# Performance work log

Hardware: AMD Instinct MI355X
Metric: run time of the kernel (lower is better)

## Reference

```python
import jax, jax.numpy as jnp
import numpy as np

N = 100000      # num nodes
E = 1600000     # num edges
DIN, DH, DOUT = 128, 64, 32
BN_EPS = 1e-5


def setup_inputs() -> dict:
    key = jax.random.key(0)
    ks = jax.random.split(key, 6)

    def xavier(k, fi, fo):
        lim = np.sqrt(6.0 / (fi + fo)).astype(np.float32)
        return jax.random.uniform(k, (fi, fo), jnp.float32, -lim, lim)

    return {
        "x": jax.random.normal(ks[0], (N, DIN), jnp.float32),
        "edge_index": jax.random.randint(ks[1], (2, E), 0, N, dtype=jnp.int32),
        "W1": xavier(ks[2], DIN, DH),
        "b1": jnp.zeros((DH,), jnp.float32),
        "gamma1": jnp.ones((DH,), jnp.float32),
        "beta1": jnp.zeros((DH,), jnp.float32),
        "W2": xavier(ks[3], DH, DOUT),
        "b2": jnp.zeros((DOUT,), jnp.float32),
    }


def _gcn_norm(edge_index, n, dtype):
    # add self-loops, then symmetric normalization deg^-1/2[src] * deg^-1/2[dst]
    loop = jnp.arange(n, dtype=edge_index.dtype)
    src = jnp.concatenate([edge_index[0], loop])
    dst = jnp.concatenate([edge_index[1], loop])
    deg = jax.ops.segment_sum(jnp.ones_like(dst, dtype=dtype), dst, num_segments=n)
    dis = 1.0 / jnp.sqrt(deg)  # deg >= 1 due to self-loops
    norm = dis[src] * dis[dst]
    return src, dst, norm


def _gcn_layer(h, W, b, src, dst, norm, n):
    h = h @ W
    msg = h[src] * norm[:, None]                       # [E+N, d] gather
    out = jax.ops.segment_sum(msg, dst, num_segments=n)  # scatter-add
    return out + b


def reference(x, edge_index, W1, b1, gamma1, beta1, W2, b2):
    src, dst, norm = _gcn_norm(edge_index, N, x.dtype)
    # layer 1: GCNConv -> BatchNorm (batch stats) -> ReLU (dropout = eval/identity)
    h = _gcn_layer(x, W1, b1, src, dst, norm, N)
    mean = h.mean(axis=0)
    var = h.var(axis=0)
    h = (h - mean) / jnp.sqrt(var + BN_EPS) * gamma1 + beta1
    h = jax.nn.relu(h)
    # layer 2: GCNConv -> node embeddings [N, DOUT]
    out = _gcn_layer(h, W2, b2, src, dst, norm, N)
    return out
```

## Files before the change

kernel.cpp:

```cpp
#include <hip/hip_runtime.h>

#define DIN 128
#define DH 64
#define DOUT 32
#define BN_EPS 1e-5f

#define BK 128
#define BKSH 7
#define NBK_MAX 784
#define G 256
#define CAP 2560
#define CCAP 3584

typedef __attribute__((ext_vector_type(8))) short short8;
typedef __attribute__((ext_vector_type(4))) float floatx4;

__device__ __forceinline__ unsigned short f2bf(float f) {
    union { float f; unsigned u; } v; v.f = f;
    unsigned r = (v.u + 0x7FFFu + ((v.u >> 16) & 1u)) >> 16;
    return (unsigned short)r;
}
__device__ __forceinline__ float bf2f(unsigned short h) {
    union { unsigned u; float f; } v; v.u = ((unsigned)h) << 16;
    return v.f;
}
__device__ __forceinline__ float lo_f(unsigned u) {
    union { unsigned u; float f; } v; v.u = u << 16;
    return v.f;
}
__device__ __forceinline__ float hi_f(unsigned u) {
    union { unsigned u; float f; } v; v.u = u & 0xFFFF0000u;
    return v.f;
}
__device__ __forceinline__ unsigned pack2bf(float lo, float hi) {
    return (unsigned)f2bf(lo) | ((unsigned)f2bf(hi) << 16);
}


__global__ __launch_bounds__(512) void hist_k(const int* __restrict__ dst, int* __restrict__ hist_g,
                                              int E, int nbk, int chunk) {
    __shared__ int hist[NBK_MAX];
    int g = blockIdx.x, tid = threadIdx.x;
    for (int b = tid; b < nbk; b += 512) hist[b] = 0;
    __syncthreads();
    int i0 = g * chunk, iend = min(i0 + chunk, E);
    for (int i = i0 + tid; i < iend; i += 512)
        atomicAdd(&hist[dst[i] >> BKSH], 1);
    __syncthreads();
    for (int b = tid; b < nbk; b += 512)
        hist_g[(size_t)g * nbk + b] = hist[b];
}


__global__ __launch_bounds__(256) void scan_k(const int* __restrict__ hist_g, int* __restrict__ rowoff,
                                              int* __restrict__ tot, int nbk) {
    __shared__ int seg[16][17];
    int tid = threadIdx.x;
    int gl = tid >> 4, bl = tid & 15;
    int b = blockIdx.x * 16 + bl;
    bool bok = b < nbk;
    int vals[16];
    int psum = 0;
    #pragma unroll
    for (int j = 0; j < 16; j++) {
        int g = gl * 16 + j;
        int v = bok ? hist_g[(size_t)g * nbk + b] : 0;
        vals[j] = v; psum += v;
    }
    seg[gl][bl] = psum;
    __syncthreads();
    #pragma unroll
    for (int off = 1; off < 16; off <<= 1) {
        int t = (gl >= off) ? seg[gl - off][bl] : 0;
        __syncthreads();
        seg[gl][bl] += t;
        __syncthreads();
    }
    int run = seg[gl][bl] - psum;
    if (gl == 15 && bok) tot[b] = seg[15][bl];
    #pragma unroll
    for (int j = 0; j < 16; j++) {
        int g = gl * 16 + j;
        if (bok) rowoff[(size_t)g * nbk + b] = run;
        run += vals[j];
    }
}


__global__ __launch_bounds__(512) void scatter_k(const int* __restrict__ src, const int* __restrict__ dst,
                                                 const int* __restrict__ rowoff,
                                                 unsigned* __restrict__ recs, int E, int nbk, int chunk) {
    __shared__ int cur[NBK_MAX];
    int g = blockIdx.x, tid = threadIdx.x;
    for (int b = tid; b < nbk; b += 512)
        cur[b] = b * CAP + rowoff[(size_t)g * nbk + b];
    __syncthreads();
    int i0 = g * chunk, iend = min(i0 + chunk, E);
    for (int i = i0 + tid; i < iend; i += 512) {
        int s = src[i], d = dst[i];
        int b = d >> BKSH;
        int slot = atomicAdd(&cur[b], 1);
        if (slot < (b + 1) * CAP)
            recs[slot] = ((unsigned)s << BKSH) | (unsigned)(d & (BK - 1));
    }
}


__global__ __launch_bounds__(512) void csr_k(const unsigned* __restrict__ recs, const int* __restrict__ tot,
                                             float* __restrict__ dis, int2* __restrict__ rpde,
                                             int* __restrict__ col, int n) {
    __shared__ int deg8[8][BK];
    __shared__ int wb[8][BK];
    __shared__ int deg[BK], sc[BK], bas[BK];
    int b = blockIdx.x, tid = threadIdx.x;
    int w = tid >> 6, lane = tid & 63;
    for (int i = tid; i < 8 * BK; i += 512) ((int*)deg8)[i] = 0;
    __syncthreads();
    int lo = b * CAP;
    int clo = b * CCAP;
    int ne = min(tot[b], CAP);
    int hi = lo + ne;
    for (int e = lo + w * 64 + lane; e < hi; e += 512)
        atomicAdd(&deg8[w][recs[e] & (BK - 1)], 1);
    __syncthreads();
    if (tid < BK) {
        int run = 0;
        #pragma unroll
        for (int ww = 0; ww < 8; ww++) { wb[ww][tid] = run; run += deg8[ww][tid]; }
        deg[tid] = run;
        sc[tid] = (run + 7) & ~7;
    }
    __syncthreads();
    for (int off = 1; off < BK; off <<= 1) {
        int t = (tid < BK && tid >= off) ? sc[tid - off] : 0;
        __syncthreads();
        if (tid < BK) sc[tid] += t;
        __syncthreads();
    }
    if (tid < BK) {
        int d = deg[tid];
        int pdeg = (d + 7) & ~7;
        int base = sc[tid] - pdeg;
        bas[tid] = base;
        int g = b * BK + tid;
        if (g < n) {
            dis[g] = rsqrtf((float)(d + 1));
            rpde[g] = make_int2(clo + base, d);
        }
        for (int j = d; j < pdeg; j++)
            col[clo + base + j] = n;
    }
    __syncthreads();
    for (int i = tid; i < 8 * BK; i += 512)
        ((int*)wb)[i] += bas[i & (BK - 1)];
    __syncthreads();
    for (int e = lo + w * 64 + lane; e < hi; e += 512) {
        unsigned r = recs[e];
        int dl = r & (BK - 1);
        int k = atomicAdd(&wb[w][dl], 1);
        col[clo + k] = (int)(r >> BKSH);
    }
}


__global__ __launch_bounds__(256) void gemm1_k(const float* __restrict__ x,
                                               const float* __restrict__ W1,
                                               const float* __restrict__ dis,
                                               unsigned short* __restrict__ h1s, int n) {
    __shared__ unsigned short xb[64][136];
    __shared__ unsigned short wt[64][136];
    int tid = threadIdx.x;
    int r0b = blockIdx.x * 64;

    for (int c = tid; c < 2048; c += 256) {
        int k = c >> 4, n4 = (c & 15) * 4;
        float4 v = ((const float4*)W1)[c];
        wt[n4 + 0][k] = f2bf(v.x);
        wt[n4 + 1][k] = f2bf(v.y);
        wt[n4 + 2][k] = f2bf(v.z);
        wt[n4 + 3][k] = f2bf(v.w);
    }
    for (int c = tid; c < 2048; c += 256) {
        int r = c >> 5, k4 = (c & 31) * 4;
        int gr = r0b + r;
        float4 v = make_float4(0.f, 0.f, 0.f, 0.f);
        if (gr < n) v = ((const float4*)x)[(gr << 5) + (k4 >> 2)];
        ushort4 o;
        o.x = f2bf(v.x); o.y = f2bf(v.y); o.z = f2bf(v.z); o.w = f2bf(v.w);
        *(ushort4*)&xb[r][k4] = o;
    }
    __syncthreads();

    int w = tid >> 6, lane = tid & 63;
    int rr = lane & 15, q = lane >> 4;
    floatx4 acc0 = {0.f, 0.f, 0.f, 0.f}, acc1 = acc0, acc2 = acc0, acc3 = acc0;
    #pragma unroll
    for (int kt = 0; kt < 4; kt++) {
        int k0 = kt * 32 + q * 8;
        short8 a  = *(const short8*)&xb[w * 16 + rr][k0];
        short8 b0 = *(const short8*)&wt[rr][k0];
        short8 b1 = *(const short8*)&wt[16 + rr][k0];
        short8 b2 = *(const short8*)&wt[32 + rr][k0];
        short8 b3 = *(const short8*)&wt[48 + rr][k0];
        acc0 = __builtin_amdgcn_mfma_f32_16x16x32_bf16(a, b0, acc0, 0, 0, 0);
        acc1 = __builtin_amdgcn_mfma_f32_16x16x32_bf16(a, b1, acc1, 0, 0, 0);
        acc2 = __builtin_amdgcn_mfma_f32_16x16x32_bf16(a, b2, acc2, 0, 0, 0);
        acc3 = __builtin_amdgcn_mfma_f32_16x16x32_bf16(a, b3, acc3, 0, 0, 0);
    }
    #pragma unroll
    for (int t = 0; t < 4; t++) {
        int gr = r0b + w * 16 + q * 4 + t;
        if (gr < n) {
            float dd = dis[gr];
            unsigned short* o = &h1s[gr * 64];
            o[rr]      = f2bf(acc0[t] * dd);
            o[16 + rr] = f2bf(acc1[t] * dd);
            o[32 + rr] = f2bf(acc2[t] * dd);
            o[48 + rr] = f2bf(acc3[t] * dd);
        } else if (gr == n) {
            unsigned short* o = &h1s[gr * 64];
            o[rr] = 0; o[16 + rr] = 0; o[32 + rr] = 0; o[48 + rr] = 0;
        }
    }
}


__global__ __launch_bounds__(256) void agg1_k(const unsigned* __restrict__ h1p,
                                              const int2* __restrict__ rpde,
                                              const int* __restrict__ col,
                                              unsigned* __restrict__ outp, int n) {
    int node = (blockIdx.x * 256 + threadIdx.x) >> 6;
    int lane = threadIdx.x & 63;
    if (node >= n) return;
    int f2 = lane & 15, eslot = lane >> 4;
    int2 rd = rpde[node];
    int e  = __builtin_amdgcn_readfirstlane(rd.x);
    int dg = __builtin_amdgcn_readfirstlane(rd.y);
    int pdg = (dg + 7) & ~7;

    const uint2* h1q = (const uint2*)h1p;
    float l0x = 0.f, h0x = 0.f, l0y = 0.f, h0y = 0.f;
    float l1x = 0.f, h1x = 0.f, l1y = 0.f, h1y = 0.f;
    int c0 = n, c1 = n;
    if (pdg > 0) { c0 = col[e + eslot]; c1 = col[e + 4 + eslot]; }
    for (int b = 0; b < pdg; b += 8) {
        uint2 u0 = h1q[c0 * 16 + f2];
        uint2 u1 = h1q[c1 * 16 + f2];
        int bn = (b + 8 < pdg) ? b + 8 : b;
        c0 = col[e + bn + eslot];
        c1 = col[e + bn + 4 + eslot];
        l0x += lo_f(u0.x); h0x += hi_f(u0.x);
        l0y += lo_f(u0.y); h0y += hi_f(u0.y);
        l1x += lo_f(u1.x); h1x += hi_f(u1.x);
        l1y += lo_f(u1.y); h1y += hi_f(u1.y);
    }
    float ax = l0x + l1x, bx = h0x + h1x;
    float ay = l0y + l1y, by = h0y + h1y;
    ax += __shfl_xor(ax, 16, 64); ax += __shfl_xor(ax, 32, 64);
    bx += __shfl_xor(bx, 16, 64); bx += __shfl_xor(bx, 32, 64);
    ay += __shfl_xor(ay, 16, 64); ay += __shfl_xor(ay, 32, 64);
    by += __shfl_xor(by, 16, 64); by += __shfl_xor(by, 32, 64);
    if (eslot == 0) {
        uint2 us = h1q[node * 16 + f2];
        float dn = rsqrtf((float)(dg + 1));
        uint2 o;
        o.x = pack2bf((ax + lo_f(us.x)) * dn, (bx + hi_f(us.x)) * dn);
        o.y = pack2bf((ay + lo_f(us.y)) * dn, (by + hi_f(us.y)) * dn);
        ((uint2*)outp)[node * 16 + f2] = o;
    }
}


__global__ __launch_bounds__(256) void bnstats_k(const unsigned short* __restrict__ agg1b,
                                                 float* __restrict__ stats, int n) {
    int f = threadIdx.x & 63, g = threadIdx.x >> 6;
    float sum = 0.f, sq = 0.f;
    for (int r = blockIdx.x * 4 + g; r < n; r += gridDim.x * 4) {
        float v = bf2f(agg1b[r * 64 + f]);
        sum += v; sq += v * v;
    }
    __shared__ float s1[4][64], s2[4][64];
    s1[g][f] = sum; s2[g][f] = sq;
    __syncthreads();
    if (g == 0) {
        sum = s1[0][f] + s1[1][f] + s1[2][f] + s1[3][f];
        sq  = s2[0][f] + s2[1][f] + s2[2][f] + s2[3][f];
        atomicAdd(&stats[f], sum);
        atomicAdd(&stats[64 + f], sq);
    }
}


__global__ __launch_bounds__(256) void gemm2_k(const unsigned short* __restrict__ agg1b,
                                               const float* __restrict__ W2,
                                               const float* __restrict__ stats,
                                               const float* __restrict__ gamma, const float* __restrict__ beta,
                                               const float* __restrict__ dis,
                                               unsigned short* __restrict__ h2s, float invn, int n) {
    __shared__ unsigned short ab[64][72];
    __shared__ unsigned short wt[32][72];
    __shared__ float s_s[64], s_t[64];
    int tid = threadIdx.x;
    int r0b = blockIdx.x * 64;
    if (tid < 64) {
        float mean = stats[tid] * invn;
        float var = stats[64 + tid] * invn - mean * mean;
        float s = gamma[tid] * rsqrtf(var + BN_EPS);
        s_s[tid] = s;
        s_t[tid] = beta[tid] - mean * s;
    }
    for (int c = tid; c < 512; c += 256) {
        int k = c >> 3, n4 = (c & 7) * 4;
        float4 v = ((const float4*)W2)[c];
        wt[n4 + 0][k] = f2bf(v.x);
        wt[n4 + 1][k] = f2bf(v.y);
        wt[n4 + 2][k] = f2bf(v.z);
        wt[n4 + 3][k] = f2bf(v.w);
    }
    __syncthreads();
    for (int c = tid; c < 512; c += 256) {
        int r = c >> 3, k0 = (c & 7) * 8;
        int gr = r0b + r;
        unsigned short tmp[8];
        if (gr < n) {
            const unsigned short* ap = &agg1b[gr * 64 + k0];
            #pragma unroll
            for (int j = 0; j < 8; j++)
                tmp[j] = f2bf(fmaxf(bf2f(ap[j]) * s_s[k0 + j] + s_t[k0 + j], 0.f));
        } else {
            #pragma unroll
            for (int j = 0; j < 8; j++) tmp[j] = 0;
        }
        *(short8*)&ab[r][k0] = *(short8*)tmp;
    }
    __syncthreads();

    int w = tid >> 6, lane = tid & 63;
    int rr = lane & 15, q = lane >> 4;
    floatx4 acc0 = {0.f, 0.f, 0.f, 0.f}, acc1 = acc0;
    #pragma unroll
    for (int kt = 0; kt < 2; kt++) {
        int k0 = kt * 32 + q * 8;
        short8 a  = *(const short8*)&ab[w * 16 + rr][k0];
        short8 b0 = *(const short8*)&wt[rr][k0];
        short8 b1 = *(const short8*)&wt[16 + rr][k0];
        acc0 = __builtin_amdgcn_mfma_f32_16x16x32_bf16(a, b0, acc0, 0, 0, 0);
        acc1 = __builtin_amdgcn_mfma_f32_16x16x32_bf16(a, b1, acc1, 0, 0, 0);
    }
    #pragma unroll
    for (int t = 0; t < 4; t++) {
        int gr = r0b + w * 16 + q * 4 + t;
        if (gr < n) {
            float dd = dis[gr];
            h2s[gr * 32 + rr]      = f2bf(acc0[t] * dd);
            h2s[gr * 32 + 16 + rr] = f2bf(acc1[t] * dd);
        } else if (gr == n) {
            h2s[gr * 32 + rr]      = 0;
            h2s[gr * 32 + 16 + rr] = 0;
        }
    }
}


__global__ __launch_bounds__(256) void agg2_k(const unsigned* __restrict__ h2p,
                                              const int2* __restrict__ rpde,
                                              const int* __restrict__ col, const float* __restrict__ b2,
                                              float* __restrict__ out, int n) {
    int wave = (blockIdx.x * 256 + threadIdx.x) >> 6;
    int lane = threadIdx.x & 63;
    int half = lane >> 5, hl = lane & 31;
    int node = wave * 2 + half;
    if (node >= n) return;
    int f2 = hl & 7, eslot = hl >> 3;
    int2 rd = rpde[node];
    int e = rd.x, dg = rd.y;
    int pdg = (dg + 7) & ~7;

    const uint2* h2q = (const uint2*)h2p;
    float l0x = 0.f, h0x = 0.f, l0y = 0.f, h0y = 0.f;
    float l1x = 0.f, h1x = 0.f, l1y = 0.f, h1y = 0.f;
    int c0 = n, c1 = n;
    if (pdg > 0) { c0 = col[e + eslot]; c1 = col[e + 4 + eslot]; }
    for (int b = 0; b < pdg; b += 8) {
        uint2 u0 = h2q[c0 * 8 + f2];
        uint2 u1 = h2q[c1 * 8 + f2];
        int bn = (b + 8 < pdg) ? b + 8 : b;
        c0 = col[e + bn + eslot];
        c1 = col[e + bn + 4 + eslot];
        l0x += lo_f(u0.x); h0x += hi_f(u0.x);
        l0y += lo_f(u0.y); h0y += hi_f(u0.y);
        l1x += lo_f(u1.x); h1x += hi_f(u1.x);
        l1y += lo_f(u1.y); h1y += hi_f(u1.y);
    }
    float ax = l0x + l1x, bx = h0x + h1x;
    float ay = l0y + l1y, by = h0y + h1y;
    ax += __shfl_xor(ax, 8, 64); ax += __shfl_xor(ax, 16, 64);
    bx += __shfl_xor(bx, 8, 64); bx += __shfl_xor(bx, 16, 64);
    ay += __shfl_xor(ay, 8, 64); ay += __shfl_xor(ay, 16, 64);
    by += __shfl_xor(by, 8, 64); by += __shfl_xor(by, 16, 64);
    if (eslot == 0) {
        uint2 us = h2q[node * 8 + f2];
        float dn = rsqrtf((float)(dg + 1));
        float4 bb = ((const float4*)b2)[f2];
        float4 o;
        o.x = (ax + lo_f(us.x)) * dn + bb.x;
        o.y = (bx + hi_f(us.x)) * dn + bb.y;
        o.z = (ay + lo_f(us.y)) * dn + bb.z;
        o.w = (by + hi_f(us.y)) * dn + bb.w;
        ((float4*)out)[node * 8 + f2] = o;
    }
}


extern "C" void kernel_launch(void* const* d_in, const int* in_sizes, int n_in,
                              void* d_out, int out_size, void* d_ws, size_t ws_size,
                              hipStream_t stream) {
    const float* x      = (const float*)d_in[0];
    const int*   ei     = (const int*)d_in[1];
    const float* W1     = (const float*)d_in[2];
    const float* gamma1 = (const float*)d_in[4];
    const float* beta1  = (const float*)d_in[5];
    const float* W2     = (const float*)d_in[6];
    const float* b2     = (const float*)d_in[7];
    float* out = (float*)d_out;

    int N = in_sizes[0] / DIN;
    int E = in_sizes[1] / 2;
    const int* src = ei;
    const int* dst = ei + E;
    int nbk = (N + BK - 1) >> BKSH;
    int chunk = (E + G - 1) / G;

    size_t off = 0;
    auto alloc = [&](size_t elems) -> void* {
        void* p = (char*)d_ws + off * 4;
        off += (elems + 127) & ~size_t(127);
        return p;
    };
    int*            hist_g = (int*)alloc((size_t)G * NBK_MAX);
    int*            rowoff = (int*)alloc((size_t)G * NBK_MAX);
    int*            tot    = (int*)alloc(NBK_MAX);
    unsigned*       recs   = (unsigned*)alloc((size_t)NBK_MAX * CAP);
    int*            col    = (int*)alloc((size_t)NBK_MAX * CCAP);
    float*          dis    = (float*)alloc(N);
    int2*           rpde   = (int2*)alloc((size_t)N * 2);
    float*          stats  = (float*)alloc(128);
    unsigned short* h1s    = (unsigned short*)alloc((size_t)(N + 1) * DH / 2);
    unsigned short* agg1b  = (unsigned short*)alloc((size_t)N * DH / 2);
    unsigned short* h2s    = h1s;

    hipMemsetAsync(stats, 0, 128 * sizeof(float), stream);

    hist_k<<<G, 512, 0, stream>>>(dst, hist_g, E, nbk, chunk);
    scan_k<<<(nbk + 15) / 16, 256, 0, stream>>>(hist_g, rowoff, tot, nbk);
    scatter_k<<<G, 512, 0, stream>>>(src, dst, rowoff, recs, E, nbk, chunk);
    csr_k<<<nbk, 512, 0, stream>>>(recs, tot, dis, rpde, col, N);

    gemm1_k<<<(N + 63) / 64, 256, 0, stream>>>(x, W1, dis, h1s, N);
    agg1_k<<<(N + 3) / 4, 256, 0, stream>>>((const unsigned*)h1s, rpde, col, (unsigned*)agg1b, N);

    bnstats_k<<<400, 256, 0, stream>>>(agg1b, stats, N);

    gemm2_k<<<(N + 63) / 64, 256, 0, stream>>>(agg1b, W2, stats, gamma1, beta1, dis, h2s,
                                               1.0f / (float)N, N);
    agg2_k<<<(N + 7) / 8, 256, 0, stream>>>((const unsigned*)h2s, rpde, col, b2, out, N);
}
```

Measured before the change: 259.0 us.

## Batch two nodes per wave and issue all gathers upfront in aggregation kernels

Both aggregation kernels now process two destination nodes per wave (or per half-wave) and issue the first 32 neighbor index loads and feature gathers for both nodes at once, before any accumulation. This replaces the old software-pipelined loop, which kept only two gathers in flight per lane, so that many more independent memory requests are outstanding to hide gather latency. A scheduling barrier stops the compiler from interleaving the loads with the adds, and a tail loop handles degrees above 32. The cost is higher register pressure and some wasted loads on padded slots, which point to the zero row.

```diff
diff --git a/kernel.cpp b/kernel.cpp
--- a/kernel.cpp
+++ b/kernel.cpp
@@ -35,6 +35,13 @@
 __device__ __forceinline__ unsigned pack2bf(float lo, float hi) {
     return (unsigned)f2bf(lo) | ((unsigned)f2bf(hi) << 16);
 }
+
+#define LOX(u) lo_f((u).x)
+#define HIX(u) hi_f((u).x)
+#define LOY(u) lo_f((u).y)
+#define HIY(u) hi_f((u).y)
+#define SUM8(F,u0,u1,u2,u3,u4,u5,u6,u7) \
+    (((F(u0)+F(u1))+(F(u2)+F(u3)))+((F(u4)+F(u5))+(F(u6)+F(u7))))
 
 
 __global__ __launch_bounds__(512) void hist_k(const int* __restrict__ dst, int* __restrict__ hist_g,
@@ -229,44 +236,122 @@
                                               const int2* __restrict__ rpde,
                                               const int* __restrict__ col,
                                               unsigned* __restrict__ outp, int n) {
-    int node = (blockIdx.x * 256 + threadIdx.x) >> 6;
+    int wv = (blockIdx.x * 256 + threadIdx.x) >> 6;
     int lane = threadIdx.x & 63;
-    if (node >= n) return;
+    int nA = wv * 2;
+    if (nA >= n) return;
+    int nB = nA + 1;
+    bool hasB = nB < n;
     int f2 = lane & 15, eslot = lane >> 4;
-    int2 rd = rpde[node];
-    int e  = __builtin_amdgcn_readfirstlane(rd.x);
-    int dg = __builtin_amdgcn_readfirstlane(rd.y);
-    int pdg = (dg + 7) & ~7;
-
     const uint2* h1q = (const uint2*)h1p;
-    float l0x = 0.f, h0x = 0.f, l0y = 0.f, h0y = 0.f;
-    float l1x = 0.f, h1x = 0.f, l1y = 0.f, h1y = 0.f;
-    int c0 = n, c1 = n;
-    if (pdg > 0) { c0 = col[e + eslot]; c1 = col[e + 4 + eslot]; }
-    for (int b = 0; b < pdg; b += 8) {
-        uint2 u0 = h1q[c0 * 16 + f2];
-        uint2 u1 = h1q[c1 * 16 + f2];
-        int bn = (b + 8 < pdg) ? b + 8 : b;
-        c0 = col[e + bn + eslot];
-        c1 = col[e + bn + 4 + eslot];
-        l0x += lo_f(u0.x); h0x += hi_f(u0.x);
-        l0y += lo_f(u0.y); h0y += hi_f(u0.y);
-        l1x += lo_f(u1.x); h1x += hi_f(u1.x);
-        l1y += lo_f(u1.y); h1y += hi_f(u1.y);
-    }
-    float ax = l0x + l1x, bx = h0x + h1x;
-    float ay = l0y + l1y, by = h0y + h1y;
-    ax += __shfl_xor(ax, 16, 64); ax += __shfl_xor(ax, 32, 64);
-    bx += __shfl_xor(bx, 16, 64); bx += __shfl_xor(bx, 32, 64);
-    ay += __shfl_xor(ay, 16, 64); ay += __shfl_xor(ay, 32, 64);
-    by += __shfl_xor(by, 16, 64); by += __shfl_xor(by, 32, 64);
+
+    int2 rdA = rpde[nA];
+    int2 rdB = rpde[hasB ? nB : nA];
+    int eA  = __builtin_amdgcn_readfirstlane(rdA.x);
+    int dgA = __builtin_amdgcn_readfirstlane(rdA.y);
+    int eB  = __builtin_amdgcn_readfirstlane(rdB.x);
+    int dgB = hasB ? __builtin_amdgcn_readfirstlane(rdB.y) : 0;
+    int pmA = ((dgA + 7) & ~7) - 1;
+    int pmB = ((dgB + 7) & ~7) - 1;
+
+    int i0 = eslot,      i1 = 4 + eslot,  i2 = 8 + eslot,  i3 = 12 + eslot;
+    int i4 = 16 + eslot, i5 = 20 + eslot, i6 = 24 + eslot, i7 = 28 + eslot;
+
+    int a0 = col[eA + min(i0, pmA)], a1 = col[eA + min(i1, pmA)];
+    int a2 = col[eA + min(i2, pmA)], a3 = col[eA + min(i3, pmA)];
+    int a4 = col[eA + min(i4, pmA)], a5 = col[eA + min(i5, pmA)];
+    int a6 = col[eA + min(i6, pmA)], a7 = col[eA + min(i7, pmA)];
+    int b0 = col[eB + min(i0, pmB)], b1 = col[eB + min(i1, pmB)];
+    int b2 = col[eB + min(i2, pmB)], b3 = col[eB + min(i3, pmB)];
+    int b4 = col[eB + min(i4, pmB)], b5 = col[eB + min(i5, pmB)];
+    int b6 = col[eB + min(i6, pmB)], b7 = col[eB + min(i7, pmB)];
+    a0 = (i0 <= pmA) ? a0 : n;  a1 = (i1 <= pmA) ? a1 : n;
+    a2 = (i2 <= pmA) ? a2 : n;  a3 = (i3 <= pmA) ? a3 : n;
+    a4 = (i4 <= pmA) ? a4 : n;  a5 = (i5 <= pmA) ? a5 : n;
+    a6 = (i6 <= pmA) ? a6 : n;  a7 = (i7 <= pmA) ? a7 : n;
+    b0 = (i0 <= pmB) ? b0 : n;  b1 = (i1 <= pmB) ? b1 : n;
+    b2 = (i2 <= pmB) ? b2 : n;  b3 = (i3 <= pmB) ? b3 : n;
+    b4 = (i4 <= pmB) ? b4 : n;  b5 = (i5 <= pmB) ? b5 : n;
+    b6 = (i6 <= pmB) ? b6 : n;  b7 = (i7 <= pmB) ? b7 : n;
+    uint2 uA0 = h1q[a0 * 16 + f2], uA1 = h1q[a1 * 16 + f2];
+    uint2 uA2 = h1q[a2 * 16 + f2], uA3 = h1q[a3 * 16 + f2];
+    uint2 uA4 = h1q[a4 * 16 + f2], uA5 = h1q[a5 * 16 + f2];
+    uint2 uA6 = h1q[a6 * 16 + f2], uA7 = h1q[a7 * 16 + f2];
+    uint2 uB0 = h1q[b0 * 16 + f2], uB1 = h1q[b1 * 16 + f2];
+    uint2 uB2 = h1q[b2 * 16 + f2], uB3 = h1q[b3 * 16 + f2];
+    uint2 uB4 = h1q[b4 * 16 + f2], uB5 = h1q[b5 * 16 + f2];
+    uint2 uB6 = h1q[b6 * 16 + f2], uB7 = h1q[b7 * 16 + f2];
+    uint2 usA = h1q[nA * 16 + f2];
+    uint2 usB = h1q[(hasB ? nB : n) * 16 + f2];
+    __builtin_amdgcn_sched_barrier(0);
+
+    float Alx = SUM8(LOX, uA0,uA1,uA2,uA3,uA4,uA5,uA6,uA7);
+    float Ahx = SUM8(HIX, uA0,uA1,uA2,uA3,uA4,uA5,uA6,uA7);
+    float Aly = SUM8(LOY, uA0,uA1,uA2,uA3,uA4,uA5,uA6,uA7);
+    float Ahy = SUM8(HIY, uA0,uA1,uA2,uA3,uA4,uA5,uA6,uA7);
+    float Blx = SUM8(LOX, uB0,uB1,uB2,uB3,uB4,uB5,uB6,uB7);
+    float Bhx = SUM8(HIX, uB0,uB1,uB2,uB3,uB4,uB5,uB6,uB7);
+    float Bly = SUM8(LOY, uB0,uB1,uB2,uB3,uB4,uB5,uB6,uB7);
+    float Bhy = SUM8(HIY, uB0,uB1,uB2,uB3,uB4,uB5,uB6,uB7);
+
+    if (pmA >= 32) {
+        for (int b = 32; b <= pmA; b += 32) {
+            int j0 = b+eslot, j1 = b+4+eslot, j2 = b+8+eslot, j3 = b+12+eslot;
+            int j4 = b+16+eslot, j5 = b+20+eslot, j6 = b+24+eslot, j7 = b+28+eslot;
+            int s0 = col[eA+min(j0,pmA)], s1 = col[eA+min(j1,pmA)];
+            int s2 = col[eA+min(j2,pmA)], s3 = col[eA+min(j3,pmA)];
+            int s4 = col[eA+min(j4,pmA)], s5 = col[eA+min(j5,pmA)];
+            int s6 = col[eA+min(j6,pmA)], s7 = col[eA+min(j7,pmA)];
+            s0=(j0<=pmA)?s0:n; s1=(j1<=pmA)?s1:n; s2=(j2<=pmA)?s2:n; s3=(j3<=pmA)?s3:n;
+            s4=(j4<=pmA)?s4:n; s5=(j5<=pmA)?s5:n; s6=(j6<=pmA)?s6:n; s7=(j7<=pmA)?s7:n;
+            uint2 v0=h1q[s0*16+f2], v1=h1q[s1*16+f2], v2=h1q[s2*16+f2], v3=h1q[s3*16+f2];
+            uint2 v4=h1q[s4*16+f2], v5=h1q[s5*16+f2], v6=h1q[s6*16+f2], v7=h1q[s7*16+f2];
+            Alx += SUM8(LOX, v0,v1,v2,v3,v4,v5,v6,v7);
+            Ahx += SUM8(HIX, v0,v1,v2,v3,v4,v5,v6,v7);
+            Aly += SUM8(LOY, v0,v1,v2,v3,v4,v5,v6,v7);
+            Ahy += SUM8(HIY, v0,v1,v2,v3,v4,v5,v6,v7);
+        }
+    }
+    if (pmB >= 32) {
+        for (int b = 32; b <= pmB; b += 32) {
+            int j0 = b+eslot, j1 = b+4+eslot, j2 = b+8+eslot, j3 = b+12+eslot;
+            int j4 = b+16+eslot, j5 = b+20+eslot, j6 = b+24+eslot, j7 = b+28+eslot;
+            int s0 = col[eB+min(j0,pmB)], s1 = col[eB+min(j1,pmB)];
+            int s2 = col[eB+min(j2,pmB)], s3 = col[eB+min(j3,pmB)];
+            int s4 = col[eB+min(j4,pmB)], s5 = col[eB+min(j5,pmB)];
+            int s6 = col[eB+min(j6,pmB)], s7 = col[eB+min(j7,pmB)];
+            s0=(j0<=pmB)?s0:n; s1=(j1<=pmB)?s1:n; s2=(j2<=pmB)?s2:n; s3=(j3<=pmB)?s3:n;
+            s4=(j4<=pmB)?s4:n; s5=(j5<=pmB)?s5:n; s6=(j6<=pmB)?s6:n; s7=(j7<=pmB)?s7:n;
+            uint2 v0=h1q[s0*16+f2], v1=h1q[s1*16+f2], v2=h1q[s2*16+f2], v3=h1q[s3*16+f2];
+            uint2 v4=h1q[s4*16+f2], v5=h1q[s5*16+f2], v6=h1q[s6*16+f2], v7=h1q[s7*16+f2];
+            Blx += SUM8(LOX, v0,v1,v2,v3,v4,v5,v6,v7);
+            Bhx += SUM8(HIX, v0,v1,v2,v3,v4,v5,v6,v7);
+            Bly += SUM8(LOY, v0,v1,v2,v3,v4,v5,v6,v7);
+            Bhy += SUM8(HIY, v0,v1,v2,v3,v4,v5,v6,v7);
+        }
+    }
+
+    Alx += __shfl_xor(Alx, 16, 64); Alx += __shfl_xor(Alx, 32, 64);
+    Ahx += __shfl_xor(Ahx, 16, 64); Ahx += __shfl_xor(Ahx, 32, 64);
+    Aly += __shfl_xor(Aly, 16, 64); Aly += __shfl_xor(Aly, 32, 64);
+    Ahy += __shfl_xor(Ahy, 16, 64); Ahy += __shfl_xor(Ahy, 32, 64);
+    Blx += __shfl_xor(Blx, 16, 64); Blx += __shfl_xor(Blx, 32, 64);
+    Bhx += __shfl_xor(Bhx, 16, 64); Bhx += __shfl_xor(Bhx, 32, 64);
+    Bly += __shfl_xor(Bly, 16, 64); Bly += __shfl_xor(Bly, 32, 64);
+    Bhy += __shfl_xor(Bhy, 16, 64); Bhy += __shfl_xor(Bhy, 32, 64);
+
     if (eslot == 0) {
-        uint2 us = h1q[node * 16 + f2];
-        float dn = rsqrtf((float)(dg + 1));
+        float dnA = rsqrtf((float)(dgA + 1));
         uint2 o;
-        o.x = pack2bf((ax + lo_f(us.x)) * dn, (bx + hi_f(us.x)) * dn);
-        o.y = pack2bf((ay + lo_f(us.y)) * dn, (by + hi_f(us.y)) * dn);
-        ((uint2*)outp)[node * 16 + f2] = o;
+        o.x = pack2bf((Alx + lo_f(usA.x)) * dnA, (Ahx + hi_f(usA.x)) * dnA);
+        o.y = pack2bf((Aly + lo_f(usA.y)) * dnA, (Ahy + hi_f(usA.y)) * dnA);
+        ((uint2*)outp)[nA * 16 + f2] = o;
+        if (hasB) {
+            float dnB = rsqrtf((float)(dgB + 1));
+            o.x = pack2bf((Blx + lo_f(usB.x)) * dnB, (Bhx + hi_f(usB.x)) * dnB);
+            o.y = pack2bf((Bly + lo_f(usB.y)) * dnB, (Bhy + hi_f(usB.y)) * dnB);
+            ((uint2*)outp)[nB * 16 + f2] = o;
+        }
     }
 }
 
@@ -366,48 +451,126 @@
                                               const int2* __restrict__ rpde,
                                               const int* __restrict__ col, const float* __restrict__ b2,
                                               float* __restrict__ out, int n) {
-    int wave = (blockIdx.x * 256 + threadIdx.x) >> 6;
+    int wv = (blockIdx.x * 256 + threadIdx.x) >> 6;
     int lane = threadIdx.x & 63;
     int half = lane >> 5, hl = lane & 31;
-    int node = wave * 2 + half;
-    if (node >= n) return;
+    int nA = wv * 4 + half * 2;
+    if (nA >= n) return;
+    int nB = nA + 1;
+    bool hasB = nB < n;
     int f2 = hl & 7, eslot = hl >> 3;
-    int2 rd = rpde[node];
-    int e = rd.x, dg = rd.y;
-    int pdg = (dg + 7) & ~7;
-
     const uint2* h2q = (const uint2*)h2p;
-    float l0x = 0.f, h0x = 0.f, l0y = 0.f, h0y = 0.f;
-    float l1x = 0.f, h1x = 0.f, l1y = 0.f, h1y = 0.f;
-    int c0 = n, c1 = n;
-    if (pdg > 0) { c0 = col[e + eslot]; c1 = col[e + 4 + eslot]; }
-    for (int b = 0; b < pdg; b += 8) {
-        uint2 u0 = h2q[c0 * 8 + f2];
-        uint2 u1 = h2q[c1 * 8 + f2];
-        int bn = (b + 8 < pdg) ? b + 8 : b;
-        c0 = col[e + bn + eslot];
-        c1 = col[e + bn + 4 + eslot];
-        l0x += lo_f(u0.x); h0x += hi_f(u0.x);
-        l0y += lo_f(u0.y); h0y += hi_f(u0.y);
-        l1x += lo_f(u1.x); h1x += hi_f(u1.x);
-        l1y += lo_f(u1.y); h1y += hi_f(u1.y);
-    }
-    float ax = l0x + l1x, bx = h0x + h1x;
-    float ay = l0y + l1y, by = h0y + h1y;
-    ax += __shfl_xor(ax, 8, 64); ax += __shfl_xor(ax, 16, 64);
-    bx += __shfl_xor(bx, 8, 64); bx += __shfl_xor(bx, 16, 64);
-    ay += __shfl_xor(ay, 8, 64); ay += __shfl_xor(ay, 16, 64);
-    by += __shfl_xor(by, 8, 64); by += __shfl_xor(by, 16, 64);
+
+    int2 rdA = rpde[nA];
+    int2 rdB = rpde[hasB ? nB : nA];
+    int eA = rdA.x, dgA = rdA.y;
+    int eB = rdB.x, dgB = hasB ? rdB.y : 0;
+    int pmA = ((dgA + 7) & ~7) - 1;
+    int pmB = ((dgB + 7) & ~7) - 1;
+
+    int i0 = eslot,      i1 = 4 + eslot,  i2 = 8 + eslot,  i3 = 12 + eslot;
+    int i4 = 16 + eslot, i5 = 20 + eslot, i6 = 24 + eslot, i7 = 28 + eslot;
+
+    int a0 = col[eA + min(i0, pmA)], a1 = col[eA + min(i1, pmA)];
+    int a2 = col[eA + min(i2, pmA)], a3 = col[eA + min(i3, pmA)];
+    int a4 = col[eA + min(i4, pmA)], a5 = col[eA + min(i5, pmA)];
+    int a6 = col[eA + min(i6, pmA)], a7 = col[eA + min(i7, pmA)];
+    int b0 = col[eB + min(i0, pmB)], b1 = col[eB + min(i1, pmB)];
+    int b2i = col[eB + min(i2, pmB)], b3 = col[eB + min(i3, pmB)];
+    int b4 = col[eB + min(i4, pmB)], b5 = col[eB + min(i5, pmB)];
+    int b6 = col[eB + min(i6, pmB)], b7 = col[eB + min(i7, pmB)];
+    a0 = (i0 <= pmA) ? a0 : n;  a1 = (i1 <= pmA) ? a1 : n;
+    a2 = (i2 <= pmA) ? a2 : n;  a3 = (i3 <= pmA) ? a3 : n;
+    a4 = (i4 <= pmA) ? a4 : n;  a5 = (i5 <= pmA) ? a5 : n;
+    a6 = (i6 <= pmA) ? a6 : n;  a7 = (i7 <= pmA) ? a7 : n;
+    b0 = (i0 <= pmB) ? b0 : n;  b1 = (i1 <= pmB) ? b1 : n;
+    b2i = (i2 <= pmB) ? b2i : n; b3 = (i3 <= pmB) ? b3 : n;
+    b4 = (i4 <= pmB) ? b4 : n;  b5 = (i5 <= pmB) ? b5 : n;
+    b6 = (i6 <= pmB) ? b6 : n;  b7 = (i7 <= pmB) ? b7 : n;
+    uint2 uA0 = h2q[a0 * 8 + f2], uA1 = h2q[a1 * 8 + f2];
+    uint2 uA2 = h2q[a2 * 8 + f2], uA3 = h2q[a3 * 8 + f2];
+    uint2 uA4 = h2q[a4 * 8 + f2], uA5 = h2q[a5 * 8 + f2];
+    uint2 uA6 = h2q[a6 * 8 + f2], uA7 = h2q[a7 * 8 + f2];
+    uint2 uB0 = h2q[b0 * 8 + f2], uB1 = h2q[b1 * 8 + f2];
+    uint2 uB2 = h2q[b2i * 8 + f2], uB3 = h2q[b3 * 8 + f2];
+    uint2 uB4 = h2q[b4 * 8 + f2], uB5 = h2q[b5 * 8 + f2];
+    uint2 uB6 = h2q[b6 * 8 + f2], uB7 = h2q[b7 * 8 + f2];
+    uint2 usA = h2q[nA * 8 + f2];
+    uint2 usB = h2q[(hasB ? nB : n) * 8 + f2];
+    __builtin_amdgcn_sched_barrier(0);
+
+    float Alx = SUM8(LOX, uA0,uA1,uA2,uA3,uA4,uA5,uA6,uA7);
+    float Ahx = SUM8(HIX, uA0,uA1,uA2,uA3,uA4,uA5,uA6,uA7);
+    float Aly = SUM8(LOY, uA0,uA1,uA2,uA3,uA4,uA5,uA6,uA7);
+    float Ahy = SUM8(HIY, uA0,uA1,uA2,uA3,uA4,uA5,uA6,uA7);
+    float Blx = SUM8(LOX, uB0,uB1,uB2,uB3,uB4,uB5,uB6,uB7);
+    float Bhx = SUM8(HIX, uB0,uB1,uB2,uB3,uB4,uB5,uB6,uB7);
+    float Bly = SUM8(LOY, uB0,uB1,uB2,uB3,uB4,uB5,uB6,uB7);
+    float Bhy = SUM8(HIY, uB0,uB1,uB2,uB3,uB4,uB5,uB6,uB7);
+
+    if (pmA >= 32) {
+        for (int b = 32; b <= pmA; b += 32) {
+            int j0=b+eslot, j1=b+4+eslot, j2=b+8+eslot, j3=b+12+eslot;
+            int j4=b+16+eslot, j5=b+20+eslot, j6=b+24+eslot, j7=b+28+eslot;
+            int s0=col[eA+min(j0,pmA)], s1=col[eA+min(j1,pmA)];
+            int s2=col[eA+min(j2,pmA)], s3=col[eA+min(j3,pmA)];
+            int s4=col[eA+min(j4,pmA)], s5=col[eA+min(j5,pmA)];
+            int s6=col[eA+min(j6,pmA)], s7=col[eA+min(j7,pmA)];
+            s0=(j0<=pmA)?s0:n; s1=(j1<=pmA)?s1:n; s2=(j2<=pmA)?s2:n; s3=(j3<=pmA)?s3:n;
+            s4=(j4<=pmA)?s4:n; s5=(j5<=pmA)?s5:n; s6=(j6<=pmA)?s6:n; s7=(j7<=pmA)?s7:n;
+            uint2 v0=h2q[s0*8+f2], v1=h2q[s1*8+f2], v2=h2q[s2*8+f2], v3=h2q[s3*8+f2];
+            uint2 v4=h2q[s4*8+f2], v5=h2q[s5*8+f2], v6=h2q[s6*8+f2], v7=h2q[s7*8+f2];
+            Alx += SUM8(LOX, v0,v1,v2,v3,v4,v5,v6,v7);
+            Ahx += SUM8(HIX, v0,v1,v2,v3,v4,v5,v6,v7);
+            Aly += SUM8(LOY, v0,v1,v2,v3,v4,v5,v6,v7);
+            Ahy += SUM8(HIY, v0,v1,v2,v3,v4,v5,v6,v7);
+        }
+    }
+    if (pmB >= 32) {
+        for (int b = 32; b <= pmB; b += 32) {
+            int j0=b+eslot, j1=b+4+eslot, j2=b+8+eslot, j3=b+12+eslot;
+            int j4=b+16+eslot, j5=b+20+eslot, j6=b+24+eslot, j7=b+28+eslot;
+            int s0=col[eB+min(j0,pmB)], s1=col[eB+min(j1,pmB)];
+            int s2=col[eB+min(j2,pmB)], s3=col[eB+min(j3,pmB)];
+            int s4=col[eB+min(j4,pmB)], s5=col[eB+min(j5,pmB)];
+            int s6=col[eB+min(j6,pmB)], s7=col[eB+min(j7,pmB)];
+            s0=(j0<=pmB)?s0:n; s1=(j1<=pmB)?s1:n; s2=(j2<=pmB)?s2:n; s3=(j3<=pmB)?s3:n;
+            s4=(j4<=pmB)?s4:n; s5=(j5<=pmB)?s5:n; s6=(j6<=pmB)?s6:n; s7=(j7<=pmB)?s7:n;
+            uint2 v0=h2q[s0*8+f2], v1=h2q[s1*8+f2], v2=h2q[s2*8+f2], v3=h2q[s3*8+f2];
+            uint2 v4=h2q[s4*8+f2], v5=h2q[s5*8+f2], v6=h2q[s6*8+f2], v7=h2q[s7*8+f2];
+            Blx += SUM8(LOX, v0,v1,v2,v3,v4,v5,v6,v7);
+            Bhx += SUM8(HIX, v0,v1,v2,v3,v4,v5,v6,v7);
+            Bly += SUM8(LOY, v0,v1,v2,v3,v4,v5,v6,v7);
+            Bhy += SUM8(HIY, v0,v1,v2,v3,v4,v5,v6,v7);
+        }
+    }
+
+    Alx += __shfl_xor(Alx, 8, 64); Alx += __shfl_xor(Alx, 16, 64);
+    Ahx += __shfl_xor(Ahx, 8, 64); Ahx += __shfl_xor(Ahx, 16, 64);
+    Aly += __shfl_xor(Aly, 8, 64); Aly += __shfl_xor(Aly, 16, 64);
+    Ahy += __shfl_xor(Ahy, 8, 64); Ahy += __shfl_xor(Ahy, 16, 64);
+    Blx += __shfl_xor(Blx, 8, 64); Blx += __shfl_xor(Blx, 16, 64);
+    Bhx += __shfl_xor(Bhx, 8, 64); Bhx += __shfl_xor(Bhx, 16, 64);
+    Bly += __shfl_xor(Bly, 8, 64); Bly += __shfl_xor(Bly, 16, 64);
+    Bhy += __shfl_xor(Bhy, 8, 64); Bhy += __shfl_xor(Bhy, 16, 64);
+
     if (eslot == 0) {
-        uint2 us = h2q[node * 8 + f2];
-        float dn = rsqrtf((float)(dg + 1));
+        float dnA = rsqrtf((float)(dgA + 1));
         float4 bb = ((const float4*)b2)[f2];
         float4 o;
-        o.x = (ax + lo_f(us.x)) * dn + bb.x;
-        o.y = (bx + hi_f(us.x)) * dn + bb.y;
-        o.z = (ay + lo_f(us.y)) * dn + bb.z;
-        o.w = (by + hi_f(us.y)) * dn + bb.w;
-        ((float4*)out)[node * 8 + f2] = o;
+        o.x = (Alx + lo_f(usA.x)) * dnA + bb.x;
+        o.y = (Ahx + hi_f(usA.x)) * dnA + bb.y;
+        o.z = (Aly + lo_f(usA.y)) * dnA + bb.z;
+        o.w = (Ahy + hi_f(usA.y)) * dnA + bb.w;
+        ((float4*)out)[nA * 8 + f2] = o;
+        if (hasB) {
+            float dnB = rsqrtf((float)(dgB + 1));
+            o.x = (Blx + lo_f(usB.x)) * dnB + bb.x;
+            o.y = (Bhx + hi_f(usB.x)) * dnB + bb.y;
+            o.z = (Bly + lo_f(usB.y)) * dnB + bb.z;
+            o.w = (Bhy + hi_f(usB.y)) * dnB + bb.w;
+            ((float4*)out)[nB * 8 + f2] = o;
+        }
     }
 }
 
@@ -457,11 +620,11 @@
     csr_k<<<nbk, 512, 0, stream>>>(recs, tot, dis, rpde, col, N);
 
     gemm1_k<<<(N + 63) / 64, 256, 0, stream>>>(x, W1, dis, h1s, N);
-    agg1_k<<<(N + 3) / 4, 256, 0, stream>>>((const unsigned*)h1s, rpde, col, (unsigned*)agg1b, N);
+    agg1_k<<<(N + 7) / 8, 256, 0, stream>>>((const unsigned*)h1s, rpde, col, (unsigned*)agg1b, N);
 
     bnstats_k<<<400, 256, 0, stream>>>(agg1b, stats, N);
 
     gemm2_k<<<(N + 63) / 64, 256, 0, stream>>>(agg1b, W2, stats, gamma1, beta1, dis, h2s,
                                                1.0f / (float)N, N);
-    agg2_k<<<(N + 7) / 8, 256, 0, stream>>>((const unsigned*)h2s, rpde, col, b2, out, N);
-}
+    agg2_k<<<(N + 15) / 16, 256, 0, stream>>>((const unsigned*)h2s, rpde, col, b2, out, N);
+}
```

After: 253.8 us. 1.02x faster.

## Split feature tables into 16-column slabs and interleave aggregation blocks by slab

Applied to the files above, without the earlier changes.

Stores the transformed node features h1, h2 and the layer-1 aggregate as separate 16-feature (32-byte) column slabs instead of row-major 64/32-wide rows. The aggregation kernels now assign each block to one slab and a subset of nodes, interleaving slab IDs across consecutive blocks so each slab's gathered working set stays small enough to remain cache-resident. Each node uses 32 lanes, with four neighbour loads issued up front before accumulation, followed by a tail loop for higher-degree nodes. In exchange, row data is read several times with narrower 32-byte gathers, the col/rpde lookups are repeated per slab, and all producer and consumer indexing has to be rewritten.

```diff
diff --git a/kernel.cpp b/kernel.cpp
--- a/kernel.cpp
+++ b/kernel.cpp
@@ -166,7 +166,7 @@
 __global__ __launch_bounds__(256) void gemm1_k(const float* __restrict__ x,
                                                const float* __restrict__ W1,
                                                const float* __restrict__ dis,
-                                               unsigned short* __restrict__ h1s, int n) {
+                                               unsigned short* __restrict__ h1s, int n, int np1) {
     __shared__ unsigned short xb[64][136];
     __shared__ unsigned short wt[64][136];
     int tid = threadIdx.x;
@@ -212,14 +212,15 @@
         int gr = r0b + w * 16 + q * 4 + t;
         if (gr < n) {
             float dd = dis[gr];
-            unsigned short* o = &h1s[gr * 64];
-            o[rr]      = f2bf(acc0[t] * dd);
-            o[16 + rr] = f2bf(acc1[t] * dd);
-            o[32 + rr] = f2bf(acc2[t] * dd);
-            o[48 + rr] = f2bf(acc3[t] * dd);
+            h1s[(size_t)0 * np1 * 16 + gr * 16 + rr] = f2bf(acc0[t] * dd);
+            h1s[(size_t)1 * np1 * 16 + gr * 16 + rr] = f2bf(acc1[t] * dd);
+            h1s[(size_t)2 * np1 * 16 + gr * 16 + rr] = f2bf(acc2[t] * dd);
+            h1s[(size_t)3 * np1 * 16 + gr * 16 + rr] = f2bf(acc3[t] * dd);
         } else if (gr == n) {
-            unsigned short* o = &h1s[gr * 64];
-            o[rr] = 0; o[16 + rr] = 0; o[32 + rr] = 0; o[48 + rr] = 0;
+            h1s[(size_t)0 * np1 * 16 + gr * 16 + rr] = 0;
+            h1s[(size_t)1 * np1 * 16 + gr * 16 + rr] = 0;
+            h1s[(size_t)2 * np1 * 16 + gr * 16 + rr] = 0;
+            h1s[(size_t)3 * np1 * 16 + gr * 16 + rr] = 0;
         }
     }
 }
@@ -228,65 +229,86 @@
 __global__ __launch_bounds__(256) void agg1_k(const unsigned* __restrict__ h1p,
                                               const int2* __restrict__ rpde,
                                               const int* __restrict__ col,
-                                              unsigned* __restrict__ outp, int n) {
-    int node = (blockIdx.x * 256 + threadIdx.x) >> 6;
+                                              unsigned* __restrict__ outp, int n, int np1, int nh) {
+    int b = blockIdx.x;
+    int slot = b & 7;
+    int q = slot >> 1, hn = slot & 1;
+    int wv = threadIdx.x >> 6;
     int lane = threadIdx.x & 63;
+    int half = lane >> 5, hl = lane & 31;
+    int f = hl & 3, eslot = hl >> 2;
+    int node = hn * nh + (b >> 3) * 8 + wv * 2 + half;
     if (node >= n) return;
-    int f2 = lane & 15, eslot = lane >> 4;
+
     int2 rd = rpde[node];
-    int e  = __builtin_amdgcn_readfirstlane(rd.x);
-    int dg = __builtin_amdgcn_readfirstlane(rd.y);
-    int pdg = (dg + 7) & ~7;
-
-    const uint2* h1q = (const uint2*)h1p;
-    float l0x = 0.f, h0x = 0.f, l0y = 0.f, h0y = 0.f;
-    float l1x = 0.f, h1x = 0.f, l1y = 0.f, h1y = 0.f;
-    int c0 = n, c1 = n;
-    if (pdg > 0) { c0 = col[e + eslot]; c1 = col[e + 4 + eslot]; }
-    for (int b = 0; b < pdg; b += 8) {
-        uint2 u0 = h1q[c0 * 16 + f2];
-        uint2 u1 = h1q[c1 * 16 + f2];
-        int bn = (b + 8 < pdg) ? b + 8 : b;
-        c0 = col[e + bn + eslot];
-        c1 = col[e + bn + 4 + eslot];
-        l0x += lo_f(u0.x); h0x += hi_f(u0.x);
-        l0y += lo_f(u0.y); h0y += hi_f(u0.y);
-        l1x += lo_f(u1.x); h1x += hi_f(u1.x);
-        l1y += lo_f(u1.y); h1y += hi_f(u1.y);
-    }
-    float ax = l0x + l1x, bx = h0x + h1x;
-    float ay = l0y + l1y, by = h0y + h1y;
-    ax += __shfl_xor(ax, 16, 64); ax += __shfl_xor(ax, 32, 64);
-    bx += __shfl_xor(bx, 16, 64); bx += __shfl_xor(bx, 32, 64);
-    ay += __shfl_xor(ay, 16, 64); ay += __shfl_xor(ay, 32, 64);
-    by += __shfl_xor(by, 16, 64); by += __shfl_xor(by, 32, 64);
+    int e = rd.x, dg = rd.y;
+    int pm = ((dg + 7) & ~7) - 1;
+
+    const uint2* qt = (const uint2*)h1p + (size_t)q * np1 * 4;
+
+    int i0 = eslot, i1 = 8 + eslot, i2 = 16 + eslot, i3 = 24 + eslot;
+    int s0 = col[e + min(i0, pm)];
+    int s1 = col[e + min(i1, pm)];
+    int s2 = col[e + min(i2, pm)];
+    int s3 = col[e + min(i3, pm)];
+    s0 = (i0 <= pm) ? s0 : n;
+    s1 = (i1 <= pm) ? s1 : n;
+    s2 = (i2 <= pm) ? s2 : n;
+    s3 = (i3 <= pm) ? s3 : n;
+    uint2 u0 = qt[s0 * 4 + f];
+    uint2 u1 = qt[s1 * 4 + f];
+    uint2 u2 = qt[s2 * 4 + f];
+    uint2 u3 = qt[s3 * 4 + f];
+    uint2 us = qt[node * 4 + f];
+    __builtin_amdgcn_sched_barrier(0);
+
+    float xl = (lo_f(u0.x) + lo_f(u1.x)) + (lo_f(u2.x) + lo_f(u3.x));
+    float xh = (hi_f(u0.x) + hi_f(u1.x)) + (hi_f(u2.x) + hi_f(u3.x));
+    float yl = (lo_f(u0.y) + lo_f(u1.y)) + (lo_f(u2.y) + lo_f(u3.y));
+    float yh = (hi_f(u0.y) + hi_f(u1.y)) + (hi_f(u2.y) + hi_f(u3.y));
+
+    if (pm >= 32) {
+        for (int bb = 32; bb <= pm; bb += 8) {
+            int s = col[e + bb + eslot];
+            uint2 u = qt[s * 4 + f];
+            xl += lo_f(u.x); xh += hi_f(u.x);
+            yl += lo_f(u.y); yh += hi_f(u.y);
+        }
+    }
+
+    xl += __shfl_xor(xl, 4, 64); xl += __shfl_xor(xl, 8, 64); xl += __shfl_xor(xl, 16, 64);
+    xh += __shfl_xor(xh, 4, 64); xh += __shfl_xor(xh, 8, 64); xh += __shfl_xor(xh, 16, 64);
+    yl += __shfl_xor(yl, 4, 64); yl += __shfl_xor(yl, 8, 64); yl += __shfl_xor(yl, 16, 64);
+    yh += __shfl_xor(yh, 4, 64); yh += __shfl_xor(yh, 8, 64); yh += __shfl_xor(yh, 16, 64);
+
     if (eslot == 0) {
-        uint2 us = h1q[node * 16 + f2];
         float dn = rsqrtf((float)(dg + 1));
         uint2 o;
-        o.x = pack2bf((ax + lo_f(us.x)) * dn, (bx + hi_f(us.x)) * dn);
-        o.y = pack2bf((ay + lo_f(us.y)) * dn, (by + hi_f(us.y)) * dn);
-        ((uint2*)outp)[node * 16 + f2] = o;
+        o.x = pack2bf((xl + lo_f(us.x)) * dn, (xh + hi_f(us.x)) * dn);
+        o.y = pack2bf((yl + lo_f(us.y)) * dn, (yh + hi_f(us.y)) * dn);
+        ((uint2*)outp)[((size_t)q * n + node) * 4 + f] = o;
     }
 }
 
 
 __global__ __launch_bounds__(256) void bnstats_k(const unsigned short* __restrict__ agg1b,
                                                  float* __restrict__ stats, int n) {
-    int f = threadIdx.x & 63, g = threadIdx.x >> 6;
+    int fidx = threadIdx.x & 63, g = threadIdx.x >> 6;
+    int qq = fidx >> 4, fi = fidx & 15;
+    const unsigned short* base = agg1b + (size_t)qq * n * 16 + fi;
     float sum = 0.f, sq = 0.f;
     for (int r = blockIdx.x * 4 + g; r < n; r += gridDim.x * 4) {
-        float v = bf2f(agg1b[r * 64 + f]);
+        float v = bf2f(base[(size_t)r * 16]);
         sum += v; sq += v * v;
     }
     __shared__ float s1[4][64], s2[4][64];
-    s1[g][f] = sum; s2[g][f] = sq;
+    s1[g][fidx] = sum; s2[g][fidx] = sq;
     __syncthreads();
     if (g == 0) {
-        sum = s1[0][f] + s1[1][f] + s1[2][f] + s1[3][f];
-        sq  = s2[0][f] + s2[1][f] + s2[2][f] + s2[3][f];
-        atomicAdd(&stats[f], sum);
-        atomicAdd(&stats[64 + f], sq);
+        sum = s1[0][fidx] + s1[1][fidx] + s1[2][fidx] + s1[3][fidx];
+        sq  = s2[0][fidx] + s2[1][fidx] + s2[2][fidx] + s2[3][fidx];
+        atomicAdd(&stats[fidx], sum);
+        atomicAdd(&stats[64 + fidx], sq);
     }
 }
 
@@ -296,7 +318,7 @@
                                                const float* __restrict__ stats,
                                                const float* __restrict__ gamma, const float* __restrict__ beta,
                                                const float* __restrict__ dis,
-                                               unsigned short* __restrict__ h2s, float invn, int n) {
+                                               unsigned short* __restrict__ h2s, float invn, int n, int np1) {
     __shared__ unsigned short ab[64][72];
     __shared__ unsigned short wt[32][72];
     __shared__ float s_s[64], s_t[64];
@@ -323,7 +345,7 @@
         int gr = r0b + r;
         unsigned short tmp[8];
         if (gr < n) {
-            const unsigned short* ap = &agg1b[gr * 64 + k0];
+            const unsigned short* ap = &agg1b[(size_t)(k0 >> 4) * n * 16 + gr * 16 + (k0 & 8)];
             #pragma unroll
             for (int j = 0; j < 8; j++)
                 tmp[j] = f2bf(fmaxf(bf2f(ap[j]) * s_s[k0 + j] + s_t[k0 + j], 0.f));
@@ -352,11 +374,11 @@
         int gr = r0b + w * 16 + q * 4 + t;
         if (gr < n) {
             float dd = dis[gr];
-            h2s[gr * 32 + rr]      = f2bf(acc0[t] * dd);
-            h2s[gr * 32 + 16 + rr] = f2bf(acc1[t] * dd);
+            h2s[(size_t)0 * np1 * 16 + gr * 16 + rr] = f2bf(acc0[t] * dd);
+            h2s[(size_t)1 * np1 * 16 + gr * 16 + rr] = f2bf(acc1[t] * dd);
         } else if (gr == n) {
-            h2s[gr * 32 + rr]      = 0;
-            h2s[gr * 32 + 16 + rr] = 0;
+            h2s[(size_t)0 * np1 * 16 + gr * 16 + rr] = 0;
+            h2s[(size_t)1 * np1 * 16 + gr * 16 + rr] = 0;
         }
     }
 }
@@ -365,49 +387,67 @@
 __global__ __launch_bounds__(256) void agg2_k(const unsigned* __restrict__ h2p,
                                               const int2* __restrict__ rpde,
                                               const int* __restrict__ col, const float* __restrict__ b2,
-                                              float* __restrict__ out, int n) {
-    int wave = (blockIdx.x * 256 + threadIdx.x) >> 6;
+                                              float* __restrict__ out, int n, int np1, int nq) {
+    int b = blockIdx.x;
+    int slot = b & 7;
+    int h = slot >> 2, qn = slot & 3;
+    int wv = threadIdx.x >> 6;
     int lane = threadIdx.x & 63;
     int half = lane >> 5, hl = lane & 31;
-    int node = wave * 2 + half;
+    int f = hl & 3, eslot = hl >> 2;
+    int node = qn * nq + (b >> 3) * 8 + wv * 2 + half;
     if (node >= n) return;
-    int f2 = hl & 7, eslot = hl >> 3;
+
     int2 rd = rpde[node];
     int e = rd.x, dg = rd.y;
-    int pdg = (dg + 7) & ~7;
-
-    const uint2* h2q = (const uint2*)h2p;
-    float l0x = 0.f, h0x = 0.f, l0y = 0.f, h0y = 0.f;
-    float l1x = 0.f, h1x = 0.f, l1y = 0.f, h1y = 0.f;
-    int c0 = n, c1 = n;
-    if (pdg > 0) { c0 = col[e + eslot]; c1 = col[e + 4 + eslot]; }
-    for (int b = 0; b < pdg; b += 8) {
-        uint2 u0 = h2q[c0 * 8 + f2];
-        uint2 u1 = h2q[c1 * 8 + f2];
-        int bn = (b + 8 < pdg) ? b + 8 : b;
-        c0 = col[e + bn + eslot];
-        c1 = col[e + bn + 4 + eslot];
-        l0x += lo_f(u0.x); h0x += hi_f(u0.x);
-        l0y += lo_f(u0.y); h0y += hi_f(u0.y);
-        l1x += lo_f(u1.x); h1x += hi_f(u1.x);
-        l1y += lo_f(u1.y); h1y += hi_f(u1.y);
-    }
-    float ax = l0x + l1x, bx = h0x + h1x;
-    float ay = l0y + l1y, by = h0y + h1y;
-    ax += __shfl_xor(ax, 8, 64); ax += __shfl_xor(ax, 16, 64);
-    bx += __shfl_xor(bx, 8, 64); bx += __shfl_xor(bx, 16, 64);
-    ay += __shfl_xor(ay, 8, 64); ay += __shfl_xor(ay, 16, 64);
-    by += __shfl_xor(by, 8, 64); by += __shfl_xor(by, 16, 64);
+    int pm = ((dg + 7) & ~7) - 1;
+
+    const uint2* ht = (const uint2*)h2p + (size_t)h * np1 * 4;
+
+    int i0 = eslot, i1 = 8 + eslot, i2 = 16 + eslot, i3 = 24 + eslot;
+    int s0 = col[e + min(i0, pm)];
+    int s1 = col[e + min(i1, pm)];
+    int s2 = col[e + min(i2, pm)];
+    int s3 = col[e + min(i3, pm)];
+    s0 = (i0 <= pm) ? s0 : n;
+    s1 = (i1 <= pm) ? s1 : n;
+    s2 = (i2 <= pm) ? s2 : n;
+    s3 = (i3 <= pm) ? s3 : n;
+    uint2 u0 = ht[s0 * 4 + f];
+    uint2 u1 = ht[s1 * 4 + f];
+    uint2 u2 = ht[s2 * 4 + f];
+    uint2 u3 = ht[s3 * 4 + f];
+    uint2 us = ht[node * 4 + f];
+    __builtin_amdgcn_sched_barrier(0);
+
+    float xl = (lo_f(u0.x) + lo_f(u1.x)) + (lo_f(u2.x) + lo_f(u3.x));
+    float xh = (hi_f(u0.x) + hi_f(u1.x)) + (hi_f(u2.x) + hi_f(u3.x));
+    float yl = (lo_f(u0.y) + lo_f(u1.y)) + (lo_f(u2.y) + lo_f(u3.y));
+    float yh = (hi_f(u0.y) + hi_f(u1.y)) + (hi_f(u2.y) + hi_f(u3.y));
+
+    if (pm >= 32) {
+        for (int bb = 32; bb <= pm; bb += 8) {
+            int s = col[e + bb + eslot];
+            uint2 u = ht[s * 4 + f];
+            xl += lo_f(u.x); xh += hi_f(u.x);
+            yl += lo_f(u.y); yh += hi_f(u.y);
+        }
+    }
+
+    xl += __shfl_xor(xl, 4, 64); xl += __shfl_xor(xl, 8, 64); xl += __shfl_xor(xl, 16, 64);
+    xh += __shfl_xor(xh, 4, 64); xh += __shfl_xor(xh, 8, 64); xh += __shfl_xor(xh, 16, 64);
+    yl += __shfl_xor(yl, 4, 64); yl += __shfl_xor(yl, 8, 64); yl += __shfl_xor(yl, 16, 64);
+    yh += __shfl_xor(yh, 4, 64); yh += __shfl_xor(yh, 8, 64); yh += __shfl_xor(yh, 16, 64);
+
     if (eslot == 0) {
-        uint2 us = h2q[node * 8 + f2];
         float dn = rsqrtf((float)(dg + 1));
-        float4 bb = ((const float4*)b2)[f2];
+        float4 bb4 = ((const float4*)b2)[h * 4 + f];
         float4 o;
-        o.x = (ax + lo_f(us.x)) * dn + bb.x;
-        o.y = (bx + hi_f(us.x)) * dn + bb.y;
-        o.z = (ay + lo_f(us.y)) * dn + bb.z;
-        o.w = (by + hi_f(us.y)) * dn + bb.w;
-        ((float4*)out)[node * 8 + f2] = o;
+        o.x = (xl + lo_f(us.x)) * dn + bb4.x;
+        o.y = (xh + hi_f(us.x)) * dn + bb4.y;
+        o.z = (yl + lo_f(us.y)) * dn + bb4.z;
+        o.w = (yh + hi_f(us.y)) * dn + bb4.w;
+        ((float4*)out)[(size_t)node * 8 + h * 4 + f] = o;
     }
 }
 
@@ -430,6 +470,7 @@
     const int* dst = ei + E;
     int nbk = (N + BK - 1) >> BKSH;
     int chunk = (E + G - 1) / G;
+    int np1 = N + 1;
 
     size_t off = 0;
     auto alloc = [&](size_t elems) -> void* {
@@ -445,7 +486,7 @@
     float*          dis    = (float*)alloc(N);
     int2*           rpde   = (int2*)alloc((size_t)N * 2);
     float*          stats  = (float*)alloc(128);
-    unsigned short* h1s    = (unsigned short*)alloc((size_t)(N + 1) * DH / 2);
+    unsigned short* h1s    = (unsigned short*)alloc((size_t)np1 * DH / 2);
     unsigned short* agg1b  = (unsigned short*)alloc((size_t)N * DH / 2);
     unsigned short* h2s    = h1s;
 
@@ -456,12 +497,20 @@
     scatter_k<<<G, 512, 0, stream>>>(src, dst, rowoff, recs, E, nbk, chunk);
     csr_k<<<nbk, 512, 0, stream>>>(recs, tot, dis, rpde, col, N);
 
-    gemm1_k<<<(N + 63) / 64, 256, 0, stream>>>(x, W1, dis, h1s, N);
-    agg1_k<<<(N + 3) / 4, 256, 0, stream>>>((const unsigned*)h1s, rpde, col, (unsigned*)agg1b, N);
+    gemm1_k<<<(N + 63) / 64, 256, 0, stream>>>(x, W1, dis, h1s, N, np1);
+
+    int nh = (N + 1) / 2;
+    int agg1_blocks = 8 * ((nh + 7) / 8);
+    agg1_k<<<agg1_blocks, 256, 0, stream>>>((const unsigned*)h1s, rpde, col, (unsigned*)agg1b,
+                                            N, np1, nh);
 
     bnstats_k<<<400, 256, 0, stream>>>(agg1b, stats, N);
 
     gemm2_k<<<(N + 63) / 64, 256, 0, stream>>>(agg1b, W2, stats, gamma1, beta1, dis, h2s,
-                                               1.0f / (float)N, N);
-    agg2_k<<<(N + 7) / 8, 256, 0, stream>>>((const unsigned*)h2s, rpde, col, b2, out, N);
-}
+                                               1.0f / (float)N, N, np1);
+
+    int nqn = (N + 3) / 4;
+    int agg2_blocks = 8 * ((nqn + 7) / 8);
+    agg2_k<<<agg2_blocks, 256, 0, stream>>>((const unsigned*)h2s, rpde, col, b2, out,
+                                            N, np1, nqn);
+}
```

New measurement: 288.7 us. 1.11x slower.
